# Optimization experiments

Hardware: AMD Instinct MI355X
Metric: run time of the kernel (lower is better)

The kernel has to match this reference:

```python
import jax, jax.numpy as jnp
import numpy as np

QMAX_ACT = 127.0  # int8 symmetric token-wise activation quant


def _dequant_weight(qweight, zeros, qstep, base_scales, step_scales):
    # qweight: [OC, IC] int in [0,16); zeros/qstep: [OC, G] int; base/step scales: [OC]
    OC, IC = qweight.shape
    G = qstep.shape[1]
    gs = IC // G
    # per (oc, g) scale reconstructed from base + quantized step decomposition
    scales = base_scales[:, None] + step_scales[:, None] * qstep.astype(jnp.float32)  # [OC, G]
    w = (qweight.reshape(OC, G, gs).astype(jnp.float32) - zeros.astype(jnp.float32)[:, :, None]) * scales[:, :, None]
    return w.reshape(OC, IC)


def _tokenwise_quant(x):
    # symmetric per-token int8 quantization
    amax = jnp.max(jnp.abs(x), axis=-1, keepdims=True)  # [B, S, 1]
    x_scales = amax / QMAX_ACT
    qx = jnp.clip(jnp.round(x / jnp.maximum(x_scales, 1e-8)), -QMAX_ACT, QMAX_ACT)
    return qx, x_scales


def setup_inputs() -> dict:
    key = jax.random.key(0)
    k1, k2, k3, k4, k5, k6 = jax.random.split(key, 6)
    B, S, IC, OC, G = 4, 2048, 4096, 4096, 32
    x = jax.random.normal(k1, (B, S, IC), dtype=jnp.float32)
    qweight = jax.random.randint(k2, (OC, IC), 0, 16, dtype=jnp.int32)
    zeros = jax.random.randint(k3, (OC, G), 0, 16, dtype=jnp.int32)
    qstep = jax.random.randint(k4, (OC, G), 0, 16, dtype=jnp.int32)
    base_scales = jax.random.uniform(k5, (OC,), dtype=jnp.float32) * 0.01 + 1e-4
    step_scales = jax.random.uniform(k6, (OC,), dtype=jnp.float32) * 0.001
    return {"x": x, "qweight": qweight, "zeros": zeros, "qstep": qstep,
            "base_scales": base_scales, "step_scales": step_scales}


def reference(x, qweight, zeros, qstep, base_scales, step_scales):
    # Faithful QuantLinear forward: token-wise int8 activation quant, then
    # GEMM against grouped int4 weight dequantized with base+step scale decomposition.
    W = _dequant_weight(qweight, zeros, qstep, base_scales, step_scales)  # [OC, IC]
    qx, x_scales = _tokenwise_quant(x)  # [B,S,IC], [B,S,1]
    out = jnp.einsum('bsi,oi->bso', qx, W) * x_scales  # fused dequant-GEMM semantics
    return out
```

## Files before the change

### kernel.cpp

```cpp
#include <hip/hip_runtime.h>
#include <hip/hip_bf16.h>

typedef int   i32x4 __attribute__((ext_vector_type(4)));
typedef float f32x4 __attribute__((ext_vector_type(4)));

constexpr int K_IC = 4096;
constexpr int N_OC = 4096;
constexpr int GROUPS = 32;

__global__ __launch_bounds__(256) void prep_kernel(const float* __restrict__ x,
                                                   const int* __restrict__ qweight,
                                                   const int* __restrict__ zeros,
                                                   const int* __restrict__ qstep,
                                                   const float* __restrict__ base_scales,
                                                   const float* __restrict__ step_scales,
                                                   char* __restrict__ qx8,
                                                   char* __restrict__ w8,
                                                   float* __restrict__ sT,
                                                   float* __restrict__ x_scales,
                                                   int M) {
    const int tid = threadIdx.x;
    if ((int)blockIdx.x < M) {
        const int m = blockIdx.x;
        const float4* xr = (const float4*)(x + (size_t)m * K_IC);
        float4 v[4];
        float amax = 0.f;
#pragma unroll
        for (int i = 0; i < 4; ++i) {
            v[i] = xr[i * 256 + tid];
            amax = fmaxf(amax, fmaxf(fmaxf(fabsf(v[i].x), fabsf(v[i].y)),
                                     fmaxf(fabsf(v[i].z), fabsf(v[i].w))));
        }
#pragma unroll
        for (int off = 32; off > 0; off >>= 1)
            amax = fmaxf(amax, __shfl_xor(amax, off, 64));
        __shared__ float wmax[4];
        if ((tid & 63) == 0) wmax[tid >> 6] = amax;
        __syncthreads();
        amax = fmaxf(fmaxf(wmax[0], wmax[1]), fmaxf(wmax[2], wmax[3]));

        const float scale = amax / 127.0f;
        if (tid == 0) x_scales[m] = scale;
        const float inv = 1.0f / fmaxf(scale, 1e-8f);

        char4* qr = (char4*)(qx8 + (size_t)m * K_IC);
#pragma unroll
        for (int i = 0; i < 4; ++i) {
            char4 o;
            o.x = (char)(int)fminf(fmaxf(rintf(v[i].x * inv), -127.f), 127.f);
            o.y = (char)(int)fminf(fmaxf(rintf(v[i].y * inv), -127.f), 127.f);
            o.z = (char)(int)fminf(fmaxf(rintf(v[i].z * inv), -127.f), 127.f);
            o.w = (char)(int)fminf(fmaxf(rintf(v[i].w * inv), -127.f), 127.f);
            qr[i * 256 + tid] = o;
        }
    } else {
        const int oc = blockIdx.x - M;
        const int4* qwr = (const int4*)(qweight + (size_t)oc * K_IC);
        char4* wr = (char4*)(w8 + (size_t)oc * K_IC);
#pragma unroll
        for (int i = 0; i < 4; ++i) {
            const int idx = i * 256 + tid;
            const int g = idx >> 5;
            const int zp = zeros[oc * GROUPS + g];
            int4 a = qwr[idx];
            char4 o;
            o.x = (char)(a.x - zp); o.y = (char)(a.y - zp);
            o.z = (char)(a.z - zp); o.w = (char)(a.w - zp);
            wr[idx] = o;
        }
        if (tid < GROUPS) {
            sT[(size_t)tid * N_OC + oc] =
                base_scales[oc] + step_scales[oc] * (float)qstep[oc * GROUPS + tid];
        }
    }
}

#define BM 128
#define BN 128
#define BK 128

__device__ inline void async16(const char* g, char* l) {
    __builtin_amdgcn_global_load_lds(
        (const __attribute__((address_space(1))) void*)g,
        (__attribute__((address_space(3))) void*)l,
        16, 0, 0);
}

__global__ __launch_bounds__(256) void gemm_kernel(const char* __restrict__ A8,
                                                   const char* __restrict__ B8,
                                                   const float* __restrict__ sT,
                                                   const float* __restrict__ x_scales,
                                                   float* __restrict__ out) {
    __shared__ __attribute__((aligned(16))) char As[BM][BK];
    __shared__ __attribute__((aligned(16))) char Bs[BN][BK];

    const int tid = threadIdx.x;
    const int lane = tid & 63;
    const int wave = tid >> 6;
    const int waveM = wave >> 1;
    const int waveN = wave & 1;
    const int bn = blockIdx.x;
    const int bm = blockIdx.y;

    f32x4 accF[4][4] = {};
    const i32x4 zeroq = {0, 0, 0, 0};

    const int rowOff = tid >> 3;
    const int srcCol = (((tid & 7) ^ ((tid >> 3) & 7))) * 16;
    const int dstCol = (tid & 7) * 16;
    const char* Aptr = A8 + (size_t)(bm * BM + rowOff) * K_IC + srcCol;
    const char* Bptr = B8 + (size_t)(bn * BN + rowOff) * K_IC + srcCol;

    const int mrow = waveM * 64 + (lane & 15);
    const int nrow = waveN * 64 + (lane & 15);
    const int q = lane >> 4;
    const int sw = lane & 7;

    const int colBase = bn * BN + waveN * 64 + (lane & 15);

    for (int g = 0; g < GROUPS; ++g) {
        const int k0 = g * BK;
#pragma unroll
        for (int it = 0; it < 4; ++it) {
            async16(Aptr + (size_t)(it * 32) * K_IC + k0, &As[rowOff + it * 32][dstCol]);
            async16(Bptr + (size_t)(it * 32) * K_IC + k0, &Bs[rowOff + it * 32][dstCol]);
        }
        float scol[4];
        const float* sg = sT + (size_t)g * N_OC + colBase;
#pragma unroll
        for (int j = 0; j < 4; ++j) scol[j] = sg[j * 16];

        __syncthreads();

        i32x4 af[2][4], bfr[2][4];
#pragma unroll
        for (int kk = 0; kk < 2; ++kk) {
            const int colA = ((kk * 4 + q) ^ sw) * 16;
#pragma unroll
            for (int i = 0; i < 4; ++i) {
                af[kk][i]  = *(const i32x4*)&As[mrow + i * 16][colA];
                bfr[kk][i] = *(const i32x4*)&Bs[nrow + i * 16][colA];
            }
        }
#pragma unroll
        for (int i = 0; i < 4; ++i)
#pragma unroll
            for (int j = 0; j < 4; ++j) {
                i32x4 p = __builtin_amdgcn_mfma_i32_16x16x64_i8(af[0][i], bfr[0][j], zeroq, 0, 0, 0);
                p = __builtin_amdgcn_mfma_i32_16x16x64_i8(af[1][i], bfr[1][j], p, 0, 0, 0);
#pragma unroll
                for (int r = 0; r < 4; ++r)
                    accF[i][j][r] += scol[j] * (float)p[r];
            }
        __syncthreads();
    }

    const int colT = lane & 15;
    const int rgrp = lane >> 4;
#pragma unroll
    for (int i = 0; i < 4; ++i) {
#pragma unroll
        for (int r = 0; r < 4; ++r) {
            const int gr = bm * BM + waveM * 64 + i * 16 + rgrp * 4 + r;
            const float sc = x_scales[gr];
#pragma unroll
            for (int j = 0; j < 4; ++j) {
                const int gc = bn * BN + waveN * 64 + j * 16 + colT;
                out[(size_t)gr * N_OC + gc] = accF[i][j][r] * sc;
            }
        }
    }
}

extern "C" void kernel_launch(void* const* d_in, const int* in_sizes, int n_in,
                              void* d_out, int out_size, void* d_ws, size_t ws_size,
                              hipStream_t stream) {
    const float* x          = (const float*)d_in[0];
    const int*   qweight    = (const int*)d_in[1];
    const int*   zeros      = (const int*)d_in[2];
    const int*   qstep      = (const int*)d_in[3];
    const float* base_scale = (const float*)d_in[4];
    const float* step_scale = (const float*)d_in[5];
    float* out = (float*)d_out;

    const int M = in_sizes[0] / K_IC;

    char* ws = (char*)d_ws;
    char*  qx8 = ws;
    char*  w8  = ws + (size_t)M * K_IC;
    float* sT  = (float*)(w8 + (size_t)N_OC * K_IC);
    float* xs  = sT + (size_t)GROUPS * N_OC;

    prep_kernel<<<M + N_OC, 256, 0, stream>>>(x, qweight, zeros, qstep,
                                              base_scale, step_scale,
                                              qx8, w8, sT, xs, M);

    dim3 grid(N_OC / BN, M / BM);
    gemm_kernel<<<grid, 256, 0, stream>>>(qx8, w8, sT, xs, out);
}
```

Baseline: 443.5 us.

## Enlarge GEMM tile to 256x256 with double-buffered LDS and block swizzle

```diff
diff --git a/kernel.cpp b/kernel.cpp
--- a/kernel.cpp
+++ b/kernel.cpp
@@ -75,8 +75,8 @@
     }
 }
 
-#define BM 128
-#define BN 128
+#define BM 256
+#define BN 256
 #define BK 128
 
 __device__ inline void async16(const char* g, char* l) {
@@ -86,82 +86,115 @@
         16, 0, 0);
 }
 
-__global__ __launch_bounds__(256) void gemm_kernel(const char* __restrict__ A8,
-                                                   const char* __restrict__ B8,
-                                                   const float* __restrict__ sT,
-                                                   const float* __restrict__ x_scales,
-                                                   float* __restrict__ out) {
-    __shared__ __attribute__((aligned(16))) char As[BM][BK];
-    __shared__ __attribute__((aligned(16))) char Bs[BN][BK];
-
-    const int tid = threadIdx.x;
+__global__ __launch_bounds__(512, 2) void gemm_kernel(const char* __restrict__ A8,
+                                                      const char* __restrict__ B8,
+                                                      const float* __restrict__ sT,
+                                                      const float* __restrict__ x_scales,
+                                                      float* __restrict__ out) {
+    __shared__ __attribute__((aligned(16))) char As[2][BM][BK];
+    __shared__ __attribute__((aligned(16))) char Bs[2][BN][BK];
+
+    const int tid  = threadIdx.x;
     const int lane = tid & 63;
     const int wave = tid >> 6;
-    const int waveM = wave >> 1;
-    const int waveN = wave & 1;
-    const int bn = blockIdx.x;
-    const int bm = blockIdx.y;
-
-    f32x4 accF[4][4] = {};
+    const int waveM = wave >> 2;
+    const int waveN = wave & 3;
+
+    const int GX   = N_OC / BN;
+    const int flat = blockIdx.y * GX + blockIdx.x;
+    const int nwg  = GX * gridDim.y;
+    int swz = flat;
+    if ((nwg & 7) == 0) swz = (flat & 7) * (nwg >> 3) + (flat >> 3);
+    const int bn = swz & (GX - 1);
+    const int bm = swz / GX;
+
+    f32x4 accF[8][4] = {};
     const i32x4 zeroq = {0, 0, 0, 0};
 
-    const int rowOff = tid >> 3;
-    const int srcCol = (((tid & 7) ^ ((tid >> 3) & 7))) * 16;
-    const int dstCol = (tid & 7) * 16;
-    const char* Aptr = A8 + (size_t)(bm * BM + rowOff) * K_IC + srcCol;
-    const char* Bptr = B8 + (size_t)(bn * BN + rowOff) * K_IC + srcCol;
-
-    const int mrow = waveM * 64 + (lane & 15);
+    const int rowInB = tid >> 3;
+    const int chunk  = tid & 7;
+    const int srcOff = ((chunk ^ (rowInB & 7)) * 16);
+    const char* Ap = A8 + (size_t)(bm * BM + rowInB) * K_IC + srcOff;
+    const char* Bp = B8 + (size_t)(bn * BN + rowInB) * K_IC + srcOff;
+
+    auto STAGE = [&](int b, int t) {
+        const int k0 = t * BK;
+#pragma unroll
+        for (int i = 0; i < 4; ++i)
+            async16(Ap + (size_t)(i * 64) * K_IC + k0, &As[b][rowInB + i * 64][chunk * 16]);
+#pragma unroll
+        for (int i = 0; i < 4; ++i)
+            async16(Bp + (size_t)(i * 64) * K_IC + k0, &Bs[b][rowInB + i * 64][chunk * 16]);
+    };
+
+    const int mrow = waveM * 128 + (lane & 15);
     const int nrow = waveN * 64 + (lane & 15);
-    const int q = lane >> 4;
-    const int sw = lane & 7;
-
+    const int q    = lane >> 4;
+    const int sw   = lane & 7;
     const int colBase = bn * BN + waveN * 64 + (lane & 15);
 
-    for (int g = 0; g < GROUPS; ++g) {
-        const int k0 = g * BK;
-#pragma unroll
-        for (int it = 0; it < 4; ++it) {
-            async16(Aptr + (size_t)(it * 32) * K_IC + k0, &As[rowOff + it * 32][dstCol]);
-            async16(Bptr + (size_t)(it * 32) * K_IC + k0, &Bs[rowOff + it * 32][dstCol]);
-        }
-        float scol[4];
-        const float* sg = sT + (size_t)g * N_OC + colBase;
-#pragma unroll
-        for (int j = 0; j < 4; ++j) scol[j] = sg[j * 16];
-
+    float scolC[4], scolN[4];
+    {
+        const float* sg = sT + colBase;
+#pragma unroll
+        for (int j = 0; j < 4; ++j) scolN[j] = sg[j * 16];
+    }
+
+    STAGE(0, 0);
+
+    for (int t = 0; t < GROUPS; ++t) {
+        const int c = t & 1;
         __syncthreads();
-
-        i32x4 af[2][4], bfr[2][4];
-#pragma unroll
-        for (int kk = 0; kk < 2; ++kk) {
-            const int colA = ((kk * 4 + q) ^ sw) * 16;
-#pragma unroll
-            for (int i = 0; i < 4; ++i) {
-                af[kk][i]  = *(const i32x4*)&As[mrow + i * 16][colA];
-                bfr[kk][i] = *(const i32x4*)&Bs[nrow + i * 16][colA];
+        if (t + 1 < GROUPS) STAGE(c ^ 1, t + 1);
+
+#pragma unroll
+        for (int j = 0; j < 4; ++j) scolC[j] = scolN[j];
+        if (t + 1 < GROUPS) {
+            const float* sg = sT + (size_t)(t + 1) * N_OC + colBase;
+#pragma unroll
+            for (int j = 0; j < 4; ++j) scolN[j] = sg[j * 16];
+        }
+
+        i32x4 bq[4][2];
+#pragma unroll
+        for (int j = 0; j < 4; ++j)
+#pragma unroll
+            for (int kk = 0; kk < 2; ++kk)
+                bq[j][kk] = *(const i32x4*)&Bs[c][nrow + j * 16][((kk * 4 + q) ^ sw) * 16];
+
+#pragma unroll
+        for (int ph = 0; ph < 4; ++ph) {
+            const int m0 = mrow + (2 * ph) * 16;
+            const int m1 = mrow + (2 * ph + 1) * 16;
+            i32x4 a0k0 = *(const i32x4*)&As[c][m0][((0 + q) ^ sw) * 16];
+            i32x4 a0k1 = *(const i32x4*)&As[c][m0][((4 + q) ^ sw) * 16];
+            i32x4 a1k0 = *(const i32x4*)&As[c][m1][((0 + q) ^ sw) * 16];
+            i32x4 a1k1 = *(const i32x4*)&As[c][m1][((4 + q) ^ sw) * 16];
+            __builtin_amdgcn_s_setprio(1);
+#pragma unroll
+            for (int j = 0; j < 4; ++j) {
+                i32x4 p = __builtin_amdgcn_mfma_i32_16x16x64_i8(a0k0, bq[j][0], zeroq, 0, 0, 0);
+                p = __builtin_amdgcn_mfma_i32_16x16x64_i8(a0k1, bq[j][1], p, 0, 0, 0);
+#pragma unroll
+                for (int r = 0; r < 4; ++r)
+                    accF[2 * ph][j][r] += scolC[j] * (float)p[r];
+                i32x4 p2 = __builtin_amdgcn_mfma_i32_16x16x64_i8(a1k0, bq[j][0], zeroq, 0, 0, 0);
+                p2 = __builtin_amdgcn_mfma_i32_16x16x64_i8(a1k1, bq[j][1], p2, 0, 0, 0);
+#pragma unroll
+                for (int r = 0; r < 4; ++r)
+                    accF[2 * ph + 1][j][r] += scolC[j] * (float)p2[r];
             }
-        }
-#pragma unroll
-        for (int i = 0; i < 4; ++i)
-#pragma unroll
-            for (int j = 0; j < 4; ++j) {
-                i32x4 p = __builtin_amdgcn_mfma_i32_16x16x64_i8(af[0][i], bfr[0][j], zeroq, 0, 0, 0);
-                p = __builtin_amdgcn_mfma_i32_16x16x64_i8(af[1][i], bfr[1][j], p, 0, 0, 0);
-#pragma unroll
-                for (int r = 0; r < 4; ++r)
-                    accF[i][j][r] += scol[j] * (float)p[r];
-            }
-        __syncthreads();
+            __builtin_amdgcn_s_setprio(0);
+        }
     }
 
     const int colT = lane & 15;
     const int rgrp = lane >> 4;
 #pragma unroll
-    for (int i = 0; i < 4; ++i) {
+    for (int i = 0; i < 8; ++i) {
 #pragma unroll
         for (int r = 0; r < 4; ++r) {
-            const int gr = bm * BM + waveM * 64 + i * 16 + rgrp * 4 + r;
+            const int gr = bm * BM + waveM * 128 + i * 16 + rgrp * 4 + r;
             const float sc = x_scales[gr];
 #pragma unroll
             for (int j = 0; j < 4; ++j) {
@@ -196,5 +229,5 @@
                                               qx8, w8, sT, xs, M);
 
     dim3 grid(N_OC / BN, M / BM);
-    gemm_kernel<<<grid, 256, 0, stream>>>(qx8, w8, sT, xs, out);
-}
+    gemm_kernel<<<grid, 512, 0, stream>>>(qx8, w8, sT, xs, out);
+}
```

Measured after the change: 462.2 us. 4.2% more time.
